# Kernel tuning notes

Hardware: AMD Instinct MI355X
Metric: run time of the kernel (lower is better)

Reference implementation:

```python
import jax, jax.numpy as jnp
import numpy as np
from jax import lax

EPS = 1e-5


def binarize(x):
    return jnp.sign(x)


def conv3x3(x, w):
    # x: NCHW, w: OIHW, stride 1, padding 1 (SAME for k=3)
    return lax.conv_general_dilated(
        x, w, window_strides=(1, 1), padding=((1, 1), (1, 1)),
        dimension_numbers=("NCHW", "OIHW", "NCHW"))


def prelu(x, a):
    # a broadcastable per-channel slope
    return jnp.where(x >= 0, x, a * x)


def bn(x, gamma, beta, axes):
    mean = jnp.mean(x, axis=axes, keepdims=True)
    var = jnp.var(x, axis=axes, keepdims=True)
    shp = [1] * x.ndim
    shp[1] = x.shape[1]
    g = gamma.reshape(shp)
    b = beta.reshape(shp)
    return (x - mean) * lax.rsqrt(var + EPS) * g + b


def setup_inputs() -> dict:
    key = jax.random.key(0)
    ks = jax.random.split(key, 8)
    B = 256
    C = [1, 64, 128]
    FC_IN = 28 * 28 * C[-1]  # 100352
    F1, F2 = 1024, 10
    inp = {
        "x": jax.random.normal(ks[0], (B, C[0], 28, 28), jnp.float32),
        "cw0": jax.random.normal(ks[1], (C[1], C[0], 3, 3), jnp.float32) * 0.1,
        "cp0": jnp.full((C[1],), 0.25, jnp.float32),
        "cg0": jnp.ones((C[1],), jnp.float32),
        "cb0": jnp.zeros((C[1],), jnp.float32),
        "cw1": jax.random.normal(ks[2], (C[2], C[1], 3, 3), jnp.float32) * 0.1,
        "cp1": jnp.full((C[2],), 0.25, jnp.float32),
        "cg1": jnp.ones((C[2],), jnp.float32),
        "cb1": jnp.zeros((C[2],), jnp.float32),
        "fw0": jax.random.normal(ks[3], (F1, FC_IN), jnp.float32) * 0.02,
        "fp0": jnp.full((F1,), 0.25, jnp.float32),
        "fg0": jnp.ones((F1,), jnp.float32),
        "fb0": jnp.zeros((F1,), jnp.float32),
        "fw1": jax.random.normal(ks[4], (F2, F1), jnp.float32) * 0.05,
        "fp1": jnp.full((F2,), 0.25, jnp.float32),
        "fg1": jnp.ones((F2,), jnp.float32),
        "fb1": jnp.zeros((F2,), jnp.float32),
        "scale": jnp.ones((1,), jnp.float32),
    }
    return inp


def reference(x, cw0, cp0, cg0, cb0, cw1, cp1, cg1, cb1,
              fw0, fp0, fg0, fb0, fw1, fp1, fg1, fb1, scale):
    # conv block 0
    h = binarize(x)
    h = conv3x3(h, jnp.sign(cw0))
    h = prelu(h, cp0[None, :, None, None])
    h = bn(h, cg0, cb0, axes=(0, 2, 3))
    # conv block 1
    h = binarize(h)
    h = conv3x3(h, jnp.sign(cw1))
    h = prelu(h, cp1[None, :, None, None])
    h = bn(h, cg1, cb1, axes=(0, 2, 3))
    # flatten
    h = h.reshape(-1, 28 * 28 * cw1.shape[0])
    # fc block 0
    h = binarize(h)
    h = h @ jnp.sign(fw0).T
    h = prelu(h, fp0[None, :])
    h = bn(h, fg0, fb0, axes=(0,))
    # fc block 1
    h = binarize(h)
    h = h @ jnp.sign(fw1).T
    h = prelu(h, fp1[None, :])
    h = bn(h, fg1, fb1, axes=(0,))
    # scale layer
    return h * scale
```

## Files before the change

kernel.cpp:

```cpp
#include <hip/hip_runtime.h>
#include <stdint.h>


static constexpr int BATCH = 256;
static constexpr int K0    = 100352;
static constexpr int KW    = 1568;
static constexpr int N1    = 1024;
static constexpr int KS2   = 49;
static constexpr int JW2   = 32;
static constexpr int SUB2  = 8;
static constexpr int NS2   = 4;
static constexpr unsigned ZCAP = 65536;

__device__ __forceinline__ float fsign(float v){
    return (v > 0.f) ? 1.f : ((v < 0.f) ? -1.f : 0.f);
}

__global__ void k_zero(int* __restrict__ p)
{
    p[threadIdx.x] = 0;
}

__global__ __launch_bounds__(256) void k_conv0(const float* __restrict__ x,
        const float* __restrict__ cw0, const float* __restrict__ cp0,
        int8_t* __restrict__ h0s, double* __restrict__ S0, double* __restrict__ Q0)
{
    __shared__ float img[30][30];
    __shared__ float redS[4][64];
    __shared__ float redQ[4][64];
    int b = blockIdx.x;
    int tid = threadIdx.x;
    for (int i = tid; i < 900; i += 256) ((float*)img)[i] = 0.f;
    __syncthreads();
    for (int i = tid; i < 784; i += 256) {
        float v = x[b*784 + i];
        img[1 + i/28][1 + i%28] = fsign(v);
    }
    __syncthreads();
    int lane = tid & 63, wv = tid >> 6;
    float wsg[9];
    #pragma unroll
    for (int t = 0; t < 9; t++) wsg[t] = fsign(cw0[lane*9 + t]);
    float a = cp0[lane];
    float accS = 0.f, accQ = 0.f;
    for (int i = 0; i < 196; i++) {
        int p = wv*196 + i;
        int y = p / 28, xx = p % 28;
        float s = 0.f;
        #pragma unroll
        for (int dy = 0; dy < 3; dy++)
            #pragma unroll
            for (int dx = 0; dx < 3; dx++)
                s += img[y+dy][xx+dx] * wsg[dy*3+dx];
        h0s[(size_t)(b*784 + p)*64 + lane] = (int8_t)(int)s;
        float v = (s >= 0.f) ? s : a*s;
        accS += v; accQ += v*v;
    }
    redS[wv][lane] = accS; redQ[wv][lane] = accQ;
    __syncthreads();
    if (tid < 64) {
        double s = (double)redS[0][tid] + redS[1][tid] + redS[2][tid] + redS[3][tid];
        double q = (double)redQ[0][tid] + redQ[1][tid] + redQ[2][tid] + redQ[3][tid];
        atomicAdd(&S0[tid], s);
        atomicAdd(&Q0[tid], q);
    }
}

__global__ void k_bnfin(const double* __restrict__ S, const double* __restrict__ Q,
        const float* __restrict__ g, const float* __restrict__ bb,
        double* __restrict__ AB, int C, double invN)
{
    int c = threadIdx.x;
    if (c >= C) return;
    double mean = S[c] * invN;
    double var  = Q[c] * invN - mean*mean;
    if (var < 0.0) var = 0.0;
    double A = (double)g[c] / sqrt(var + 1e-5);
    AB[c]     = A;
    AB[C + c] = (double)bb[c] - mean*A;
}

__global__ __launch_bounds__(256) void k_pack_h0(const int8_t* __restrict__ h0s,
        const float* __restrict__ cp0, const double* __restrict__ AB,
        uint64_t* __restrict__ hp)
{
    int idx = blockIdx.x * 4 + (threadIdx.x >> 6);
    int lane = threadIdx.x & 63;
    float s = (float)h0s[(size_t)idx*64 + lane];
    float a = cp0[lane];
    float v = (s >= 0.f) ? s : a*s;
    double t = fma((double)v, AB[lane], AB[64 + lane]);
    uint64_t m = __ballot(t < 0.0);
    if (lane == 0) hp[idx] = m;
}

__global__ __launch_bounds__(256) void k_pack_w1(const float* __restrict__ cw1,
        uint64_t* __restrict__ wn1, uint64_t* __restrict__ wnz1)
{
    int idx = blockIdx.x*4 + (threadIdx.x >> 6);
    int lane = threadIdx.x & 63;
    int oc = idx / 9, t = idx % 9;
    float w = cw1[oc*576 + lane*9 + t];
    uint64_t n = __ballot(w < 0.f);
    uint64_t z = __ballot(w != 0.f);
    if (lane == 0) { wn1[idx] = n; wnz1[idx] = z; }
}

__global__ __launch_bounds__(256) void k_conv1(const uint64_t* __restrict__ hp,
        const uint64_t* __restrict__ wn1, const uint64_t* __restrict__ wnz1,
        const float* __restrict__ cp1, int16_t* __restrict__ h1s,
        double* __restrict__ S1, double* __restrict__ Q1)
{
    __shared__ float lS[4][8];
    __shared__ float lQ[4][8];
    int bid = blockIdx.x;
    int ocg = bid & 15;
    int ptg = (bid >> 4) & 3;
    int b   = bid >> 6;
    int wv = threadIdx.x >> 6, lane = threadIdx.x & 63;
    int pt = ptg*4 + wv;
    bool active = (pt < 13);
    int p = active ? (pt*64 + lane) : 0;
    bool pvalid = active && (p < 784);
    int y = p / 28, xx = p % 28;
    uint64_t nb[9]; unsigned vmask = 0;
    #pragma unroll
    for (int dy = 0; dy < 3; dy++)
        #pragma unroll
        for (int dx = 0; dx < 3; dx++) {
            int t = dy*3+dx;
            int yy = y + dy - 1, xv = xx + dx - 1;
            bool ok = (yy >= 0 && yy < 28 && xv >= 0 && xv < 28);
            nb[t] = hp[b*784 + (ok ? (yy*28+xv) : 0)];
            if (ok) vmask |= 1u << t;
        }
    #pragma unroll
    for (int o = 0; o < 8; o++) {
        int oc = ocg*8 + o;
        int base = oc*9;
        int acc = 0;
        #pragma unroll
        for (int t = 0; t < 9; t++) {
            uint64_t wn = wn1[base+t], wz = wnz1[base+t];
            if (vmask & (1u<<t))
                acc += (int)__popcll(wz) - 2*(int)__popcll((nb[t] ^ wn) & wz);
        }
        if (pvalid) h1s[((size_t)b*128 + oc)*784 + p] = (int16_t)acc;
        float pr = cp1[oc];
        float v = pvalid ? ((acc >= 0) ? (float)acc : pr*(float)acc) : 0.f;
        float s = v, q = v*v;
        #pragma unroll
        for (int off = 32; off; off >>= 1) {
            s += __shfl_xor(s, off);
            q += __shfl_xor(q, off);
        }
        if (lane == 0) { lS[wv][o] = s; lQ[wv][o] = q; }
    }
    __syncthreads();
    if (threadIdx.x < 8) {
        int o = threadIdx.x;
        double s = (double)lS[0][o] + lS[1][o] + lS[2][o] + lS[3][o];
        double q = (double)lQ[0][o] + lQ[1][o] + lQ[2][o] + lQ[3][o];
        atomicAdd(&S1[ocg*8 + o], s);
        atomicAdd(&Q1[ocg*8 + o], q);
    }
}

__global__ __launch_bounds__(256) void k_pack_a0(const int16_t* __restrict__ h1s,
        const float* __restrict__ cp1, const double* __restrict__ AB,
        uint64_t* __restrict__ ap_t)
{
    int bb = blockIdx.x / 392;
    int jg = blockIdx.x % 392;
    int j = jg*4 + (threadIdx.x >> 6);
    int lane = threadIdx.x & 63;
    int k = j*64 + lane;
    int oc = k / 784;
    int p  = k - oc*784;
    float s = (float)h1s[((size_t)bb*128 + oc)*784 + p];
    float a = cp1[oc];
    float v = (s >= 0.f) ? s : a*s;
    double t = fma((double)v, AB[oc], AB[128+oc]);
    uint64_t m = __ballot(t < 0.0);
    if (lane == 0) ap_t[(size_t)j*256 + bb] = m;
}

__global__ __launch_bounds__(256) void k_pack_w0(const float* __restrict__ fw0,
        uint64_t* __restrict__ wp_t, unsigned* __restrict__ zcnt,
        uint64_t* __restrict__ zlist)
{
    int ng = blockIdx.x >> 3;
    int ch = blockIdx.x & 7;
    int wv = threadIdx.x >> 6, lane = threadIdx.x & 63;
    int n0 = ng*8;
    int jw0 = ch*196 + wv*49;
    const float* base = fw0 + (size_t)n0*K0 + lane;
    for (int t = 0; t < 49; ++t) {
        int jw = jw0 + t;
        size_t koff = (size_t)jw*64;
        uint64_t nb[8], zb[8];
        #pragma unroll
        for (int r = 0; r < 8; ++r) {
            float w = base[(size_t)r*K0 + koff];
            nb[r] = __ballot(w < 0.f);
            zb[r] = __ballot(w == 0.f);
        }
        uint64_t mine = nb[0];
        #pragma unroll
        for (int r = 1; r < 8; ++r) mine = (lane == r) ? nb[r] : mine;
        if (lane < 8) wp_t[(size_t)jw*N1 + n0 + lane] = mine;
        if (lane == 0) {
            #pragma unroll
            for (int r = 0; r < 8; ++r) if (zb[r]) {
                unsigned id = atomicAdd(zcnt, 1u);
                if (id < ZCAP) {
                    zlist[2*id]   = ((uint64_t)(unsigned)(n0+r) << 32) | (unsigned)jw;
                    zlist[2*id+1] = zb[r];
                }
            }
        }
    }
}

__global__ __launch_bounds__(256) void k_fc0g(const uint64_t* __restrict__ wp_t,
        const uint64_t* __restrict__ ap_t, int16_t* __restrict__ pcpart)
{
    __shared__ uint64_t wL[SUB2][32];
    __shared__ uint64_t apL[SUB2][256];
    int nt = blockIdx.x & 31;
    int ks = blockIdx.x >> 5;
    int tid = threadIdx.x;
    int bq = tid & 31;
    int nq = tid >> 5;
    int n0 = nt*32;
    int pc[8][4];
    #pragma unroll
    for (int i=0;i<8;i++)
        #pragma unroll
        for (int k=0;k<4;k++) pc[i][k]=0;
    int jbase = ks*JW2;
    for (int c = 0; c < NS2; c++) {
        int j0 = jbase + c*SUB2;
        #pragma unroll
        for (int r = 0; r < SUB2; r++)
            apL[r][tid] = ap_t[(size_t)(j0 + r)*256 + tid];
        {
            int jj = tid >> 5, n = tid & 31;
            wL[jj][n] = wp_t[(size_t)(j0 + jj)*N1 + n0 + n];
        }
        __syncthreads();
        #pragma unroll
        for (int jj = 0; jj < SUB2; jj++) {
            uint64_t aw[8], ww[4];
            #pragma unroll
            for (int i = 0; i < 8; i++) aw[i] = apL[jj][bq + 32*i];
            #pragma unroll
            for (int k = 0; k < 4; k++) ww[k] = wL[jj][nq + 8*k];
            #pragma unroll
            for (int i = 0; i < 8; i++)
                #pragma unroll
                for (int k = 0; k < 4; k++)
                    pc[i][k] += (int)__popcll(aw[i] ^ ww[k]);
        }
        __syncthreads();
    }
    #pragma unroll
    for (int k = 0; k < 4; k++) {
        int n = n0 + nq + 8*k;
        #pragma unroll
        for (int i = 0; i < 8; i++)
            pcpart[((size_t)ks*N1 + n)*BATCH + (bq + 32*i)] = (int16_t)pc[i][k];
    }
}

__global__ __launch_bounds__(256) void k_fc0ep(const int16_t* __restrict__ pcpart,
        const unsigned* __restrict__ zcnt, const uint64_t* __restrict__ zlist,
        const uint64_t* __restrict__ ap_t, const float* __restrict__ fp0,
        const float* __restrict__ fg0, const float* __restrict__ fb0,
        float* __restrict__ af)
{
    int n = blockIdx.x, b = threadIdx.x;
    int pc = 0;
    #pragma unroll
    for (int ks = 0; ks < KS2; ks++) pc += (int)pcpart[((size_t)ks*N1 + n)*BATCH + b];
    int s = K0 - 2*pc;
    unsigned cnt = *zcnt; if (cnt > ZCAP) cnt = ZCAP;
    for (unsigned e = 0; e < cnt; ++e) {
        uint64_t key = zlist[2*e];
        if ((int)(key >> 32) == n) {
            uint64_t zm = zlist[2*e+1];
            uint64_t a = ap_t[(size_t)(key & 0xffffffffu)*256 + b];
            s += 2*(int)__popcll(a & zm) - (int)__popcll(zm);
        }
    }
    float a = fp0[n];
    float v = (s >= 0) ? (float)s : a*(float)s;
    __shared__ double rs[256], rq[256];
    rs[b] = v; rq[b] = (double)v*(double)v;
    __syncthreads();
    for (int off=128; off>0; off>>=1){
        if (b<off){ rs[b]+=rs[b+off]; rq[b]+=rq[b+off]; }
        __syncthreads();
    }
    __shared__ double AB[2];
    if (b == 0) {
        double mean = rs[0] / 256.0;
        double var = rq[0] / 256.0 - mean*mean;
        if (var < 0.0) var = 0.0;
        double A = (double)fg0[n] / sqrt(var + 1e-5);
        AB[0] = A; AB[1] = (double)fb0[n] - mean*A;
    }
    __syncthreads();
    double t = fma((double)v, AB[0], AB[1]);
    af[(size_t)n*256 + b] = (t > 0.0) ? 1.f : ((t < 0.0) ? -1.f : 0.f);
}

__global__ __launch_bounds__(256) void k_fc1a(const float* __restrict__ af,
        const float* __restrict__ fw1, float* __restrict__ part9)
{
    __shared__ float swL[10][32];
    int ks = blockIdx.x, b = threadIdx.x;
    for (int i = b; i < 320; i += 256) {
        int j = i / 32, kk = i % 32;
        swL[j][kk] = fsign(fw1[j*1024 + ks*32 + kk]);
    }
    __syncthreads();
    float acc[10];
    #pragma unroll
    for (int j=0;j<10;j++) acc[j]=0.f;
    for (int kk = 0; kk < 32; kk++) {
        float a = af[(size_t)(ks*32+kk)*256 + b];
        #pragma unroll
        for (int j=0;j<10;j++) acc[j] += a * swL[j][kk];
    }
    #pragma unroll
    for (int j=0;j<10;j++) part9[((size_t)ks*256 + b)*10 + j] = acc[j];
}

__global__ __launch_bounds__(256) void k_fc1b(const float* __restrict__ part9,
        const float* __restrict__ fp1, const float* __restrict__ fg1,
        const float* __restrict__ fb1, const float* __restrict__ scale,
        float* __restrict__ out)
{
    int b = threadIdx.x;
    float v[10];
    #pragma unroll
    for (int j=0;j<10;j++) v[j]=0.f;
    for (int ks=0; ks<32; ks++)
        #pragma unroll
        for (int j=0;j<10;j++) v[j] += part9[((size_t)ks*256+b)*10 + j];
    #pragma unroll
    for (int j=0;j<10;j++){
        float a = fp1[j];
        v[j] = (v[j] >= 0.f) ? v[j] : a*v[j];
    }
    __shared__ double sv[256];
    __shared__ double AB[2][10];
    for (int j=0;j<10;j++){
        sv[b] = (double)v[j];
        __syncthreads();
        for (int off=128;off>0;off>>=1){ if(b<off) sv[b]+=sv[b+off]; __syncthreads(); }
        double mean = sv[0]/256.0;
        __syncthreads();
        double d = (double)v[j]-mean;
        sv[b] = d*d;
        __syncthreads();
        for (int off=128;off>0;off>>=1){ if(b<off) sv[b]+=sv[b+off]; __syncthreads(); }
        if (b==0){
            double var = sv[0]/256.0;
            double A = (double)fg1[j]/sqrt(var+1e-5);
            AB[0][j]=A; AB[1][j]=(double)fb1[j] - mean*A;
        }
        __syncthreads();
    }
    float sc = scale[0];
    #pragma unroll
    for (int j=0;j<10;j++)
        out[b*10+j] = (float)fma((double)v[j], AB[0][j], AB[1][j]) * sc;
}

extern "C" void kernel_launch(void* const* d_in, const int* in_sizes, int n_in,
                              void* d_out, int out_size, void* d_ws, size_t ws_size,
                              hipStream_t stream)
{
    const float* x    = (const float*)d_in[0];
    const float* cw0  = (const float*)d_in[1];
    const float* cp0  = (const float*)d_in[2];
    const float* cg0  = (const float*)d_in[3];
    const float* cb0  = (const float*)d_in[4];
    const float* cw1  = (const float*)d_in[5];
    const float* cp1  = (const float*)d_in[6];
    const float* cg1  = (const float*)d_in[7];
    const float* cb1  = (const float*)d_in[8];
    const float* fw0  = (const float*)d_in[9];
    const float* fp0  = (const float*)d_in[10];
    const float* fg0  = (const float*)d_in[11];
    const float* fb0  = (const float*)d_in[12];
    const float* fw1  = (const float*)d_in[13];
    const float* fp1  = (const float*)d_in[14];
    const float* fg1  = (const float*)d_in[15];
    const float* fb1  = (const float*)d_in[16];
    const float* scale= (const float*)d_in[17];

    char* ws = (char*)d_ws;
    size_t off = 0;
    auto alloc = [&](size_t bytes)->char* {
        char* r = ws + off; off = (off + bytes + 255) & ~(size_t)255; return r; };

    double*   S0    = (double*)alloc(64*8);
    double*   Q0    = (double*)alloc(64*8);
    double*   S1    = (double*)alloc(128*8);
    double*   Q1    = (double*)alloc(128*8);
    unsigned* zcnt  = (unsigned*)alloc(256);
    double*   A0B0  = (double*)alloc(128*8);
    double*   A1B1  = (double*)alloc(256*8);
    int8_t*   h0s   = (int8_t*)alloc((size_t)256*784*64);
    uint64_t* hp    = (uint64_t*)alloc((size_t)256*784*8);
    int16_t*  h1s   = (int16_t*)alloc((size_t)256*128*784*2);
    uint64_t* ap_t  = (uint64_t*)alloc((size_t)KW*256*8);
    uint64_t* wn1   = (uint64_t*)alloc(1152*8);
    uint64_t* wnz1  = (uint64_t*)alloc(1152*8);
    uint64_t* wp_t  = (uint64_t*)alloc((size_t)KW*N1*8);
    int16_t*  pcpart= (int16_t*)alloc((size_t)KS2*N1*BATCH*2);
    float*    af    = (float*)alloc((size_t)1024*256*4);
    float*    part9 = (float*)alloc((size_t)32*256*10*4);
    uint64_t* zlist = (uint64_t*)alloc((size_t)ZCAP*16);
    (void)ws_size; (void)in_sizes; (void)n_in; (void)out_size;

    k_zero   <<<1,    1024, 0, stream>>>((int*)d_ws);
    k_conv0  <<<256,   256, 0, stream>>>(x, cw0, cp0, h0s, S0, Q0);
    k_bnfin  <<<1,      64, 0, stream>>>(S0, Q0, cg0, cb0, A0B0, 64, 1.0/200704.0);
    k_pack_h0<<<50176, 256, 0, stream>>>(h0s, cp0, A0B0, hp);
    k_pack_w1<<<288,   256, 0, stream>>>(cw1, wn1, wnz1);
    k_conv1  <<<16384, 256, 0, stream>>>(hp, wn1, wnz1, cp1, h1s, S1, Q1);
    k_bnfin  <<<1,     128, 0, stream>>>(S1, Q1, cg1, cb1, A1B1, 128, 1.0/200704.0);
    k_pack_a0<<<100352,256, 0, stream>>>(h1s, cp1, A1B1, ap_t);
    k_pack_w0<<<1024,  256, 0, stream>>>(fw0, wp_t, zcnt, zlist);
    k_fc0g   <<<KS2*32,256, 0, stream>>>(wp_t, ap_t, pcpart);
    k_fc0ep  <<<1024,  256, 0, stream>>>(pcpart, zcnt, zlist, ap_t, fp0, fg0, fb0, af);
    k_fc1a   <<<32,    256, 0, stream>>>(af, fw1, part9);
    k_fc1b   <<<1,     256, 0, stream>>>(part9, fp1, fg1, fb1, scale, (float*)d_out);
}
```

Measured before the change: 403.8 us.

## Rework packing kernels: LUT-based h0 pack, vectorized a0/w0 packing, row-major weight bits

Replaces the per-channel double-precision BN threshold in the h0 pack with a 19-entry bitmask lookup table per channel, so one thread packs a whole pixel from vectorized int8 loads. The a0 and w0 packers now use vector loads and emit several ballot words per wave. The weight bits are stored row-major per output neuron, and fc0g loads them once into a padded shared tile. The zeroing kernel is folded into k_pack_w1 to save a launch. The aim is fewer blocks, less memory traffic and fewer launches, at the cost of changed layouts that must stay consistent with k_fc0ep's use of zlist indices.

Result: faster. 355.1 us (-12.1%).

```diff
diff --git a/kernel.cpp b/kernel.cpp
--- a/kernel.cpp
+++ b/kernel.cpp
@@ -16,9 +16,20 @@
     return (v > 0.f) ? 1.f : ((v < 0.f) ? -1.f : 0.f);
 }
 
-__global__ void k_zero(int* __restrict__ p)
-{
-    p[threadIdx.x] = 0;
+__global__ __launch_bounds__(256) void k_pack_w1(const float* __restrict__ cw1,
+        uint64_t* __restrict__ wn1, uint64_t* __restrict__ wnz1,
+        int* __restrict__ zero_region)
+{
+    if (blockIdx.x == 0) {
+        for (int i = threadIdx.x; i < 832; i += 256) zero_region[i] = 0;
+    }
+    int idx = blockIdx.x*4 + (threadIdx.x >> 6);
+    int lane = threadIdx.x & 63;
+    int oc = idx / 9, t = idx % 9;
+    float w = cw1[oc*576 + lane*9 + t];
+    uint64_t n = __ballot(w < 0.f);
+    uint64_t z = __ballot(w != 0.f);
+    if (lane == 0) { wn1[idx] = n; wnz1[idx] = z; }
 }
 
 __global__ __launch_bounds__(256) void k_conv0(const float* __restrict__ x,
@@ -64,6 +75,26 @@
         atomicAdd(&S0[tid], s);
         atomicAdd(&Q0[tid], q);
     }
+}
+
+__global__ void k_bnfin0(const double* __restrict__ S, const double* __restrict__ Q,
+        const float* __restrict__ g, const float* __restrict__ bb,
+        const float* __restrict__ cp0, unsigned* __restrict__ lut)
+{
+    int c = threadIdx.x;
+    double mean = S[c] * (1.0/200704.0);
+    double var  = Q[c] * (1.0/200704.0) - mean*mean;
+    if (var < 0.0) var = 0.0;
+    double A = (double)g[c] / sqrt(var + 1e-5);
+    double B = (double)bb[c] - mean*A;
+    float a = cp0[c];
+    unsigned m = 0;
+    for (int s = -9; s <= 9; ++s) {
+        float v = (s >= 0) ? (float)s : a*(float)s;
+        double t = fma((double)v, A, B);
+        if (t < 0.0) m |= 1u << (s + 9);
+    }
+    lut[c] = m;
 }
 
 __global__ void k_bnfin(const double* __restrict__ S, const double* __restrict__ Q,
@@ -81,29 +112,30 @@
 }
 
 __global__ __launch_bounds__(256) void k_pack_h0(const int8_t* __restrict__ h0s,
-        const float* __restrict__ cp0, const double* __restrict__ AB,
-        uint64_t* __restrict__ hp)
-{
-    int idx = blockIdx.x * 4 + (threadIdx.x >> 6);
-    int lane = threadIdx.x & 63;
-    float s = (float)h0s[(size_t)idx*64 + lane];
-    float a = cp0[lane];
-    float v = (s >= 0.f) ? s : a*s;
-    double t = fma((double)v, AB[lane], AB[64 + lane]);
-    uint64_t m = __ballot(t < 0.0);
-    if (lane == 0) hp[idx] = m;
-}
-
-__global__ __launch_bounds__(256) void k_pack_w1(const float* __restrict__ cw1,
-        uint64_t* __restrict__ wn1, uint64_t* __restrict__ wnz1)
-{
-    int idx = blockIdx.x*4 + (threadIdx.x >> 6);
-    int lane = threadIdx.x & 63;
-    int oc = idx / 9, t = idx % 9;
-    float w = cw1[oc*576 + lane*9 + t];
-    uint64_t n = __ballot(w < 0.f);
-    uint64_t z = __ballot(w != 0.f);
-    if (lane == 0) { wn1[idx] = n; wnz1[idx] = z; }
+        const unsigned* __restrict__ lut, uint64_t* __restrict__ hp)
+{
+    __shared__ unsigned l[64];
+    int tid = threadIdx.x;
+    if (tid < 64) l[tid] = lut[tid];
+    __syncthreads();
+    int pixel = blockIdx.x*256 + tid;
+    const int4* p4 = (const int4*)(h0s + (size_t)pixel*64);
+    int4 va = p4[0], vb = p4[1], vc = p4[2], vd = p4[3];
+    int wa[16] = {va.x,va.y,va.z,va.w, vb.x,vb.y,vb.z,vb.w,
+                  vc.x,vc.y,vc.z,vc.w, vd.x,vd.y,vd.z,vd.w};
+    unsigned lo = 0, hi = 0;
+    #pragma unroll
+    for (int wi = 0; wi < 16; ++wi) {
+        unsigned w = (unsigned)wa[wi];
+        #pragma unroll
+        for (int c2 = 0; c2 < 4; ++c2) {
+            int ch = wi*4 + c2;
+            int s = (int)(signed char)(w >> (8*c2));
+            unsigned bit = (l[ch] >> (s + 9)) & 1u;
+            if (ch < 32) lo |= bit << ch; else hi |= bit << (ch - 32);
+        }
+    }
+    hp[pixel] = ((uint64_t)hi << 32) | lo;
 }
 
 __global__ __launch_bounds__(256) void k_conv1(const uint64_t* __restrict__ hp,
@@ -170,84 +202,98 @@
         const float* __restrict__ cp1, const double* __restrict__ AB,
         uint64_t* __restrict__ ap_t)
 {
-    int bb = blockIdx.x / 392;
-    int jg = blockIdx.x % 392;
-    int j = jg*4 + (threadIdx.x >> 6);
+    int blk = blockIdx.x;
+    int b  = blk / 98;
+    int qg = blk % 98;
+    int wv = threadIdx.x >> 6, lane = threadIdx.x & 63;
+    int q  = qg*4 + wv;
+    int k0 = q*256 + lane*4;
+    short4 sv = *(const short4*)(h1s + (size_t)b*K0 + k0);
+    int oc = k0 / 784;
+    double A = AB[oc], B = AB[128 + oc];
+    float a = cp1[oc];
+    int ss[4] = {sv.x, sv.y, sv.z, sv.w};
+    uint64_t words[4];
+    #pragma unroll
+    for (int c = 0; c < 4; ++c) {
+        float s = (float)ss[c];
+        float v = (s >= 0.f) ? s : a*s;
+        double t = fma((double)v, A, B);
+        words[c] = __ballot(t < 0.0);
+    }
+    if (lane == 0) {
+        #pragma unroll
+        for (int c = 0; c < 4; ++c)
+            ap_t[(size_t)(4*q + c)*256 + b] = words[c];
+    }
+}
+
+__global__ __launch_bounds__(256) void k_pack_w0(const float* __restrict__ fw0,
+        uint64_t* __restrict__ wp, unsigned* __restrict__ zcnt,
+        uint64_t* __restrict__ zlist)
+{
+    int n   = blockIdx.x >> 1;
+    int oct = (blockIdx.x & 1)*4 + (threadIdx.x >> 6);
     int lane = threadIdx.x & 63;
-    int k = j*64 + lane;
-    int oc = k / 784;
-    int p  = k - oc*784;
-    float s = (float)h1s[((size_t)bb*128 + oc)*784 + p];
-    float a = cp1[oc];
-    float v = (s >= 0.f) ? s : a*s;
-    double t = fma((double)v, AB[oc], AB[128+oc]);
-    uint64_t m = __ballot(t < 0.0);
-    if (lane == 0) ap_t[(size_t)j*256 + bb] = m;
-}
-
-__global__ __launch_bounds__(256) void k_pack_w0(const float* __restrict__ fw0,
-        uint64_t* __restrict__ wp_t, unsigned* __restrict__ zcnt,
-        uint64_t* __restrict__ zlist)
-{
-    int ng = blockIdx.x >> 3;
-    int ch = blockIdx.x & 7;
-    int wv = threadIdx.x >> 6, lane = threadIdx.x & 63;
-    int n0 = ng*8;
-    int jw0 = ch*196 + wv*49;
-    const float* base = fw0 + (size_t)n0*K0 + lane;
+    const float* src = fw0 + (size_t)n*K0 + (size_t)oct*49*256 + lane*4;
+    uint64_t* dst = wp + (size_t)n*KW + (size_t)oct*49*4;
     for (int t = 0; t < 49; ++t) {
-        int jw = jw0 + t;
-        size_t koff = (size_t)jw*64;
-        uint64_t nb[8], zb[8];
-        #pragma unroll
-        for (int r = 0; r < 8; ++r) {
-            float w = base[(size_t)r*K0 + koff];
-            nb[r] = __ballot(w < 0.f);
-            zb[r] = __ballot(w == 0.f);
-        }
-        uint64_t mine = nb[0];
-        #pragma unroll
-        for (int r = 1; r < 8; ++r) mine = (lane == r) ? nb[r] : mine;
-        if (lane < 8) wp_t[(size_t)jw*N1 + n0 + lane] = mine;
+        float4 w = *(const float4*)(src + t*256);
+        uint64_t g0 = __ballot(w.x < 0.f);
+        uint64_t g1 = __ballot(w.y < 0.f);
+        uint64_t g2 = __ballot(w.z < 0.f);
+        uint64_t g3 = __ballot(w.w < 0.f);
+        uint64_t z0 = __ballot(w.x == 0.f);
+        uint64_t z1 = __ballot(w.y == 0.f);
+        uint64_t z2 = __ballot(w.z == 0.f);
+        uint64_t z3 = __ballot(w.w == 0.f);
         if (lane == 0) {
+            ulonglong2 lo{g0, g1}, hi{g2, g3};
+            *(ulonglong2*)(dst + t*4)     = lo;
+            *(ulonglong2*)(dst + t*4 + 2) = hi;
+            uint64_t zz[4] = {z0, z1, z2, z3};
             #pragma unroll
-            for (int r = 0; r < 8; ++r) if (zb[r]) {
+            for (int c = 0; c < 4; ++c) if (zz[c]) {
                 unsigned id = atomicAdd(zcnt, 1u);
                 if (id < ZCAP) {
-                    zlist[2*id]   = ((uint64_t)(unsigned)(n0+r) << 32) | (unsigned)jw;
-                    zlist[2*id+1] = zb[r];
+                    unsigned j = (unsigned)((oct*49 + t)*4 + c);
+                    zlist[2*id]   = ((uint64_t)(unsigned)n << 32) | j;
+                    zlist[2*id+1] = zz[c];
                 }
             }
         }
     }
 }
 
-__global__ __launch_bounds__(256) void k_fc0g(const uint64_t* __restrict__ wp_t,
+__global__ __launch_bounds__(256) void k_fc0g(const uint64_t* __restrict__ wp,
         const uint64_t* __restrict__ ap_t, int16_t* __restrict__ pcpart)
 {
-    __shared__ uint64_t wL[SUB2][32];
+    __shared__ uint64_t wT[32][33];
     __shared__ uint64_t apL[SUB2][256];
     int nt = blockIdx.x & 31;
     int ks = blockIdx.x >> 5;
     int tid = threadIdx.x;
     int bq = tid & 31;
     int nq = tid >> 5;
-    int n0 = nt*32;
+    int n0 = nt*32, j0 = ks*JW2;
+    {
+        int row = tid >> 3;
+        int wo  = (tid & 7) * 4;
+        const uint64_t* src = wp + (size_t)(n0 + row)*KW + j0 + wo;
+        ulonglong2 v0 = *(const ulonglong2*)(src);
+        ulonglong2 v1 = *(const ulonglong2*)(src + 2);
+        wT[row][wo+0] = v0.x; wT[row][wo+1] = v0.y;
+        wT[row][wo+2] = v1.x; wT[row][wo+3] = v1.y;
+    }
     int pc[8][4];
     #pragma unroll
-    for (int i=0;i<8;i++)
-        #pragma unroll
-        for (int k=0;k<4;k++) pc[i][k]=0;
-    int jbase = ks*JW2;
+    for (int i = 0; i < 8; i++)
+        #pragma unroll
+        for (int k = 0; k < 4; k++) pc[i][k] = 0;
     for (int c = 0; c < NS2; c++) {
-        int j0 = jbase + c*SUB2;
         #pragma unroll
         for (int r = 0; r < SUB2; r++)
-            apL[r][tid] = ap_t[(size_t)(j0 + r)*256 + tid];
-        {
-            int jj = tid >> 5, n = tid & 31;
-            wL[jj][n] = wp_t[(size_t)(j0 + jj)*N1 + n0 + n];
-        }
+            apL[r][tid] = ap_t[(size_t)(j0 + c*SUB2 + r)*256 + tid];
         __syncthreads();
         #pragma unroll
         for (int jj = 0; jj < SUB2; jj++) {
@@ -255,7 +301,7 @@
             #pragma unroll
             for (int i = 0; i < 8; i++) aw[i] = apL[jj][bq + 32*i];
             #pragma unroll
-            for (int k = 0; k < 4; k++) ww[k] = wL[jj][nq + 8*k];
+            for (int k = 0; k < 4; k++) ww[k] = wT[nq + 8*k][c*8 + jj];
             #pragma unroll
             for (int i = 0; i < 8; i++)
                 #pragma unroll
@@ -412,7 +458,7 @@
     double*   S1    = (double*)alloc(128*8);
     double*   Q1    = (double*)alloc(128*8);
     unsigned* zcnt  = (unsigned*)alloc(256);
-    double*   A0B0  = (double*)alloc(128*8);
+    unsigned* lut0  = (unsigned*)alloc(64*4);
     double*   A1B1  = (double*)alloc(256*8);
     int8_t*   h0s   = (int8_t*)alloc((size_t)256*784*64);
     uint64_t* hp    = (uint64_t*)alloc((size_t)256*784*8);
@@ -420,23 +466,22 @@
     uint64_t* ap_t  = (uint64_t*)alloc((size_t)KW*256*8);
     uint64_t* wn1   = (uint64_t*)alloc(1152*8);
     uint64_t* wnz1  = (uint64_t*)alloc(1152*8);
-    uint64_t* wp_t  = (uint64_t*)alloc((size_t)KW*N1*8);
+    uint64_t* wp    = (uint64_t*)alloc((size_t)N1*KW*8);
     int16_t*  pcpart= (int16_t*)alloc((size_t)KS2*N1*BATCH*2);
     float*    af    = (float*)alloc((size_t)1024*256*4);
     float*    part9 = (float*)alloc((size_t)32*256*10*4);
     uint64_t* zlist = (uint64_t*)alloc((size_t)ZCAP*16);
     (void)ws_size; (void)in_sizes; (void)n_in; (void)out_size;
 
-    k_zero   <<<1,    1024, 0, stream>>>((int*)d_ws);
+    k_pack_w1<<<288,   256, 0, stream>>>(cw1, wn1, wnz1, (int*)d_ws);
     k_conv0  <<<256,   256, 0, stream>>>(x, cw0, cp0, h0s, S0, Q0);
-    k_bnfin  <<<1,      64, 0, stream>>>(S0, Q0, cg0, cb0, A0B0, 64, 1.0/200704.0);
-    k_pack_h0<<<50176, 256, 0, stream>>>(h0s, cp0, A0B0, hp);
-    k_pack_w1<<<288,   256, 0, stream>>>(cw1, wn1, wnz1);
+    k_bnfin0 <<<1,      64, 0, stream>>>(S0, Q0, cg0, cb0, cp0, lut0);
+    k_pack_h0<<<784,   256, 0, stream>>>(h0s, lut0, hp);
     k_conv1  <<<16384, 256, 0, stream>>>(hp, wn1, wnz1, cp1, h1s, S1, Q1);
     k_bnfin  <<<1,     128, 0, stream>>>(S1, Q1, cg1, cb1, A1B1, 128, 1.0/200704.0);
-    k_pack_a0<<<100352,256, 0, stream>>>(h1s, cp1, A1B1, ap_t);
-    k_pack_w0<<<1024,  256, 0, stream>>>(fw0, wp_t, zcnt, zlist);
-    k_fc0g   <<<KS2*32,256, 0, stream>>>(wp_t, ap_t, pcpart);
+    k_pack_a0<<<256*98,256, 0, stream>>>(h1s, cp1, A1B1, ap_t);
+    k_pack_w0<<<2048,  256, 0, stream>>>(fw0, wp, zcnt, zlist);
+    k_fc0g   <<<KS2*32,256, 0, stream>>>(wp, ap_t, pcpart);
     k_fc0ep  <<<1024,  256, 0, stream>>>(pcpart, zcnt, zlist, ap_t, fp0, fg0, fb0, af);
     k_fc1a   <<<32,    256, 0, stream>>>(af, fw1, part9);
     k_fc1b   <<<1,     256, 0, stream>>>(part9, fp1, fg1, fb1, scale, (float*)d_out);
```
